# Kernel optimization log

Measured on AMD Instinct MI355X. Metric: run time of the kernel, lower is better.

The kernel has to match this reference:

```python
import jax, jax.numpy as jnp
import numpy as np

HIDDEN_NUMS = 512  # 2H = 1024, 4H = 2048


def setup_inputs() -> dict:
    key = jax.random.key(0)
    k1, k2, k3 = jax.random.split(key, 3)
    B, S, T, H2 = 32, 1024, 64, 2 * HIDDEN_NUMS
    target_hidden_states = jax.random.normal(k1, (B, T, H2), dtype=jnp.float32)
    hidden_states = jax.random.normal(k2, (B, S, H2), dtype=jnp.float32)
    # original uses RandomUniform(-0.01, 0.01)
    trans_W = jax.random.uniform(k3, (4 * HIDDEN_NUMS, H2), dtype=jnp.float32, minval=-0.01, maxval=0.01)
    trans_b = jnp.zeros((H2,), dtype=jnp.float32)
    return {
        'target_hidden_states': target_hidden_states,
        'hidden_states': hidden_states,
        'trans_W': trans_W,
        'trans_b': trans_b,
    }


def reference(target_hidden_states, hidden_states, trans_W, trans_b):
    # Vectorized form of the per-timestep while_loop (no cross-step recurrence):
    # scores[b,s,t] = <hidden[b,s], target[b,t]>
    scores = jnp.einsum('bsd,btd->bst', hidden_states, target_hidden_states)
    attn = jax.nn.softmax(scores, axis=-1)                      # (B, S, T)
    ti = jnp.einsum('bst,btd->bsd', attn, target_hidden_states)  # (B, S, 2H)
    cat = jnp.concatenate([hidden_states, ti], axis=-1)         # (B, S, 4H)
    hi_new = jnp.tanh(jnp.einsum('bsf,fd->bsd', cat, trans_W) + trans_b)
    return hi_new + hidden_states  # lf_layer residual
```

## Files before the change

kernel.cpp:

```cpp
#include <hip/hip_runtime.h>
#include <hip/hip_bf16.h>

#define BB 32
#define SS 1024
#define TT 64
#define HD 1024
#define FF 2048
#define MM (BB*SS)

typedef __attribute__((ext_vector_type(4))) float f32x4;
typedef __attribute__((ext_vector_type(8))) short bf16x8;

__device__ __forceinline__ unsigned short f2bf(float f) {
  __hip_bfloat16 h = __float2bfloat16(f);
  return __builtin_bit_cast(unsigned short, h);
}

__device__ __forceinline__ void gll16(const void* g, void* l) {
  __builtin_amdgcn_global_load_lds(
      (const __attribute__((address_space(1))) void*)g,
      (__attribute__((address_space(3))) void*)l, 16, 0, 0);
}

__global__ void cvt_bf16_kernel(const float* __restrict__ x,
                                unsigned short* __restrict__ y, int n4) {
  int stride = gridDim.x * blockDim.x;
  for (int i = blockIdx.x * blockDim.x + threadIdx.x; i < n4; i += stride) {
    float4 v = reinterpret_cast<const float4*>(x)[i];
    ushort4 o;
    o.x = f2bf(v.x); o.y = f2bf(v.y); o.z = f2bf(v.z); o.w = f2bf(v.w);
    reinterpret_cast<ushort4*>(y)[i] = o;
  }
}

__global__ void tcvt_kernel(const float* __restrict__ in,
                            unsigned short* __restrict__ out, int R, int C) {
  __shared__ float tile[32][33];
  const int bz = blockIdx.z;
  const float* ip = in + (size_t)bz * R * C;
  unsigned short* op = out + (size_t)bz * R * C;
  const int c0 = blockIdx.x * 32, r0 = blockIdx.y * 32;
  const int tx = threadIdx.x, ty = threadIdx.y;
#pragma unroll
  for (int j = 0; j < 4; ++j)
    tile[ty + j * 8][tx] = ip[(size_t)(r0 + ty + j * 8) * C + c0 + tx];
  __syncthreads();
#pragma unroll
  for (int j = 0; j < 4; ++j)
    op[(size_t)(c0 + ty + j * 8) * R + r0 + tx] = f2bf(tile[tx][ty + j * 8]);
}

__global__ __launch_bounds__(256) void attn_kernel(
    const unsigned short* __restrict__ hid_bf,
    const unsigned short* __restrict__ tgt_bf,
    const unsigned short* __restrict__ tgtT_bf,
    unsigned short* __restrict__ ti_bf)
{
  __shared__ unsigned short Qs[64 * 32];
  __shared__ unsigned short Ks[64 * 32];
  __shared__ unsigned short Ps[64 * 72];

  const int tid = threadIdx.x;
  const int w = tid >> 6, l = tid & 63;
  const int lrow = l & 15, lk = l >> 4;
  const int b = blockIdx.y;
  const int sbase = blockIdx.x * 64;

  const size_t hbase = ((size_t)b * SS + sbase) * HD;
  const size_t tbase = (size_t)b * TT * HD;
  const int srow = tid >> 2;
  const int scol = (tid & 3) * 8;

  f32x4 accs[4] = {};
  for (int kt = 0; kt < 32; ++kt) {
    const int kk = kt * 32;
    gll16(hid_bf + hbase + (size_t)srow * HD + kk + scol, Qs + w * 512);
    gll16(tgt_bf + tbase + (size_t)srow * HD + kk + scol, Ks + w * 512);
    __syncthreads();
    bf16x8 a = *reinterpret_cast<const bf16x8*>(&Qs[(w * 16 + lrow) * 32 + lk * 8]);
#pragma unroll
    for (int ct = 0; ct < 4; ++ct) {
      bf16x8 bb = *reinterpret_cast<const bf16x8*>(&Ks[(ct * 16 + lrow) * 32 + lk * 8]);
      accs[ct] = __builtin_amdgcn_mfma_f32_16x16x32_bf16(a, bb, accs[ct], 0, 0, 0);
    }
    __syncthreads();
  }

  float p[4][4];
#pragma unroll
  for (int j = 0; j < 4; ++j) {
    float mx = fmaxf(fmaxf(accs[0][j], accs[1][j]), fmaxf(accs[2][j], accs[3][j]));
#pragma unroll
    for (int d = 1; d < 16; d <<= 1) mx = fmaxf(mx, __shfl_xor(mx, d, 64));
    float sum = 0.f;
#pragma unroll
    for (int ct = 0; ct < 4; ++ct) { p[ct][j] = __expf(accs[ct][j] - mx); sum += p[ct][j]; }
#pragma unroll
    for (int d = 1; d < 16; d <<= 1) sum += __shfl_xor(sum, d, 64);
    float inv = 1.f / sum;
#pragma unroll
    for (int ct = 0; ct < 4; ++ct) p[ct][j] *= inv;
  }
#pragma unroll
  for (int j = 0; j < 4; ++j)
#pragma unroll
    for (int ct = 0; ct < 4; ++ct)
      Ps[(w * 16 + lk * 4 + j) * 72 + ct * 16 + lrow] = f2bf(p[ct][j]);
  __syncthreads();

  const size_t tTbase = (size_t)b * HD * TT;
  for (int chunk = 0; chunk < 16; ++chunk) {
    const int colbase = chunk * 64;
    f32x4 acco[4] = {};
#pragma unroll
    for (int kk2 = 0; kk2 < 2; ++kk2) {
      bf16x8 a = *reinterpret_cast<const bf16x8*>(&Ps[(w * 16 + lrow) * 72 + kk2 * 32 + lk * 8]);
#pragma unroll
      for (int ct = 0; ct < 4; ++ct) {
        const unsigned short* gp =
            tgtT_bf + tTbase + (size_t)(colbase + ct * 16 + lrow) * TT + kk2 * 32 + lk * 8;
        bf16x8 bb = *reinterpret_cast<const bf16x8*>(gp);
        acco[ct] = __builtin_amdgcn_mfma_f32_16x16x32_bf16(a, bb, acco[ct], 0, 0, 0);
      }
    }
#pragma unroll
    for (int ct = 0; ct < 4; ++ct)
#pragma unroll
      for (int j = 0; j < 4; ++j)
        ti_bf[hbase + (size_t)(w * 16 + lk * 4 + j) * HD + colbase + ct * 16 + lrow] =
            f2bf(acco[ct][j]);
  }
}


__global__ __launch_bounds__(512) void gemm_kernel(
    const unsigned short* __restrict__ hid_bf,
    const unsigned short* __restrict__ ti_bf,
    const unsigned short* __restrict__ Wt_bf,
    const float* __restrict__ bias,
    float* __restrict__ out)
{
  __shared__ unsigned short lds[65536];

  const int tid = threadIdx.x;
  const int w = tid >> 6, l = tid & 63;
  const int wm = w >> 2, wn = w & 3;
  const int lrow = l & 15, lk = l >> 4;

  const int orig = blockIdx.y * 4 + blockIdx.x;
  const int lid = (orig & 7) * 64 + (orig >> 3);
  const int nbase = (lid & 3) * 256;
  const int mbase = (lid >> 2) * 256;

  const int srow8 = w * 8 + (l >> 3);
  const int scol = ((l & 7) ^ (l >> 3)) << 3;

  const int ck0 = ((lk)     ^ (lrow & 7)) << 3;
  const int ck1 = ((4 + lk) ^ (lrow & 7)) << 3;

#define STAGE_A(s, bsel, h) do {                                               \
    const int k0_ = (s) * 64;                                                  \
    const unsigned short* p_ = (k0_ < 1024) ? (hid_bf + k0_)                   \
                                            : (ti_bf + (k0_ - 1024));          \
    _Pragma("unroll")                                                          \
    for (int rd_ = 0; rd_ < 2; ++rd_)                                          \
      gll16(p_ + (size_t)(mbase + (h) * 128 + rd_ * 64 + srow8) * HD + scol,   \
            lds + (bsel) * 32768 + (h) * 8192 + rd_ * 4096 + w * 512);         \
  } while (0)

#define STAGE_B(s, bsel, h) do {                                               \
    const int k0_ = (s) * 64;                                                  \
    _Pragma("unroll")                                                          \
    for (int rd_ = 0; rd_ < 2; ++rd_)                                          \
      gll16(Wt_bf + (size_t)(nbase + (h) * 128 + rd_ * 64 + srow8) * FF        \
                  + k0_ + scol,                                                \
            lds + (bsel) * 32768 + 16384 + (h) * 8192 + rd_ * 4096 + w * 512); \
  } while (0)

#define PH_MID do {                                                            \
    __builtin_amdgcn_s_barrier();                                              \
    __builtin_amdgcn_s_setprio(1);                                             \
  } while (0)

#define PH_END do {                                                            \
    __builtin_amdgcn_s_setprio(0);                                             \
    __builtin_amdgcn_sched_barrier(0);                                         \
    __builtin_amdgcn_s_barrier();                                              \
  } while (0)

  f32x4 acc[8][4] = {};
  bf16x8 aR[4][2], bR[4][2];

  STAGE_A(0, 0, 0); STAGE_A(0, 0, 1);
  STAGE_B(0, 0, 0); STAGE_B(0, 0, 1);
  STAGE_B(1, 1, 0); STAGE_B(1, 1, 1);
  asm volatile("s_waitcnt vmcnt(4)" ::: "memory");
  __builtin_amdgcn_sched_barrier(0);
  __builtin_amdgcn_s_barrier();

#define TILE(tt, c) do {                                                       \
    const int sa_ = ((tt) + 1 > 31) ? 31 : (tt) + 1;                           \
    const int sb_ = ((tt) + 2 > 31) ? 31 : (tt) + 2;                           \
    const int abase_ = (c) * 32768 + wm * 8192 + lrow * 64;                    \
    const int bbase_ = (c) * 32768 + 16384 + (wn >> 1) * 8192                  \
                       + ((wn & 1) * 64 + lrow) * 64;                          \
         \
    _Pragma("unroll")                                                          \
    for (int m_ = 0; m_ < 4; ++m_) {                                           \
      aR[m_][0] = *(const bf16x8*)(lds + abase_ + m_ * 1024 + ck0);            \
      aR[m_][1] = *(const bf16x8*)(lds + abase_ + m_ * 1024 + ck1);            \
    }                                                                          \
    _Pragma("unroll")                                                          \
    for (int n_ = 0; n_ < 2; ++n_) {                                           \
      bR[n_][0] = *(const bf16x8*)(lds + bbase_ + n_ * 1024 + ck0);            \
      bR[n_][1] = *(const bf16x8*)(lds + bbase_ + n_ * 1024 + ck1);            \
    }                                                                          \
    STAGE_A(sa_, 1 - (c), 0);                                                  \
    PH_MID;                                                                    \
    _Pragma("unroll")                                                          \
    for (int m_ = 0; m_ < 4; ++m_)                                             \
      _Pragma("unroll")                                                        \
      for (int n_ = 0; n_ < 2; ++n_) {                                         \
        acc[m_][n_] = __builtin_amdgcn_mfma_f32_16x16x32_bf16(                 \
            aR[m_][0], bR[n_][0], acc[m_][n_], 0, 0, 0);                       \
        acc[m_][n_] = __builtin_amdgcn_mfma_f32_16x16x32_bf16(                 \
            aR[m_][1], bR[n_][1], acc[m_][n_], 0, 0, 0);                       \
      }                                                                        \
    PH_END;                                                                    \
                  \
    _Pragma("unroll")                                                          \
    for (int n_ = 2; n_ < 4; ++n_) {                                           \
      bR[n_][0] = *(const bf16x8*)(lds + bbase_ + n_ * 1024 + ck0);            \
      bR[n_][1] = *(const bf16x8*)(lds + bbase_ + n_ * 1024 + ck1);            \
    }                                                                          \
    STAGE_A(sa_, 1 - (c), 1);                                                  \
    PH_MID;                                                                    \
    _Pragma("unroll")                                                          \
    for (int m_ = 0; m_ < 4; ++m_)                                             \
      _Pragma("unroll")                                                        \
      for (int n_ = 2; n_ < 4; ++n_) {                                         \
        acc[m_][n_] = __builtin_amdgcn_mfma_f32_16x16x32_bf16(                 \
            aR[m_][0], bR[n_][0], acc[m_][n_], 0, 0, 0);                       \
        acc[m_][n_] = __builtin_amdgcn_mfma_f32_16x16x32_bf16(                 \
            aR[m_][1], bR[n_][1], acc[m_][n_], 0, 0, 0);                       \
      }                                                                        \
    PH_END;                                                                    \
     \
    _Pragma("unroll")                                                          \
    for (int m_ = 0; m_ < 4; ++m_) {                                           \
      aR[m_][0] = *(const bf16x8*)(lds + abase_ + (m_ + 4) * 1024 + ck0);      \
      aR[m_][1] = *(const bf16x8*)(lds + abase_ + (m_ + 4) * 1024 + ck1);      \
    }                                                                          \
    STAGE_B(sb_, (c), 0);                                                      \
    PH_MID;                                                                    \
    _Pragma("unroll")                                                          \
    for (int m_ = 0; m_ < 4; ++m_)                                             \
      _Pragma("unroll")                                                        \
      for (int n_ = 0; n_ < 2; ++n_) {                                         \
        acc[m_ + 4][n_] = __builtin_amdgcn_mfma_f32_16x16x32_bf16(             \
            aR[m_][0], bR[n_][0], acc[m_ + 4][n_], 0, 0, 0);                   \
        acc[m_ + 4][n_] = __builtin_amdgcn_mfma_f32_16x16x32_bf16(             \
            aR[m_][1], bR[n_][1], acc[m_ + 4][n_], 0, 0, 0);                   \
      }                                                                        \
    PH_END;                                                                    \
       \
    STAGE_B(sb_, (c), 1);                                                      \
    PH_MID;                                                                    \
    _Pragma("unroll")                                                          \
    for (int m_ = 0; m_ < 4; ++m_)                                             \
      _Pragma("unroll")                                                        \
      for (int n_ = 2; n_ < 4; ++n_) {                                         \
        acc[m_ + 4][n_] = __builtin_amdgcn_mfma_f32_16x16x32_bf16(             \
            aR[m_][0], bR[n_][0], acc[m_ + 4][n_], 0, 0, 0);                   \
        acc[m_ + 4][n_] = __builtin_amdgcn_mfma_f32_16x16x32_bf16(             \
            aR[m_][1], bR[n_][1], acc[m_ + 4][n_], 0, 0, 0);                   \
      }                                                                        \
    __builtin_amdgcn_s_setprio(0);                                             \
    asm volatile("s_waitcnt vmcnt(4)" ::: "memory");                           \
    __builtin_amdgcn_sched_barrier(0);                                         \
    __builtin_amdgcn_s_barrier();                                              \
  } while (0)

  for (int tt = 0; tt < 32; tt += 2) {
    TILE(tt, 0);
    TILE(tt + 1, 1);
  }
#undef TILE
#undef PH_MID
#undef PH_END
#undef STAGE_A
#undef STAGE_B

#pragma unroll
  for (int m = 0; m < 8; ++m) {
    const int row = mbase + wm * 128 + m * 16 + lk * 4;
#pragma unroll
    for (int n = 0; n < 4; ++n) {
      const int col = nbase + wn * 64 + n * 16 + lrow;
      const float bv = bias[col];
#pragma unroll
      for (int j = 0; j < 4; ++j) {
        float x = acc[m][n][j] + bv;
        float xc = fminf(fmaxf(x, -15.f), 15.f);
        float e2 = __expf(2.f * xc);
        float th = (e2 - 1.f) / (e2 + 1.f);
        size_t oi = (size_t)(row + j) * HD + col;
        unsigned int u = ((unsigned int)hid_bf[oi]) << 16;
        out[oi] = th + __builtin_bit_cast(float, u);
      }
    }
  }
}

extern "C" void kernel_launch(void* const* d_in, const int* in_sizes, int n_in,
                              void* d_out, int out_size, void* d_ws, size_t ws_size,
                              hipStream_t stream) {
  const float* tgt  = (const float*)d_in[0];
  const float* hid  = (const float*)d_in[1];
  const float* W    = (const float*)d_in[2];
  const float* bias = (const float*)d_in[3];
  float* out = (float*)d_out;

  char* ws = (char*)d_ws;
  unsigned short* hid_bf  = (unsigned short*)(ws);
  unsigned short* ti_bf   = (unsigned short*)(ws + 67108864);
  unsigned short* tgt_bf  = (unsigned short*)(ws + 134217728);
  unsigned short* tgtT_bf = (unsigned short*)(ws + 138412032);
  unsigned short* Wt_bf   = (unsigned short*)(ws + 142606336);

  cvt_bf16_kernel<<<2048, 256, 0, stream>>>(hid, hid_bf, (BB * SS * HD) / 4);
  cvt_bf16_kernel<<<512, 256, 0, stream>>>(tgt, tgt_bf, (BB * TT * HD) / 4);
  tcvt_kernel<<<dim3(HD / 32, TT / 32, BB), dim3(32, 8), 0, stream>>>(tgt, tgtT_bf, TT, HD);
  tcvt_kernel<<<dim3(HD / 32, FF / 32, 1), dim3(32, 8), 0, stream>>>(W, Wt_bf, FF, HD);
  attn_kernel<<<dim3(SS / 64, BB), 256, 0, stream>>>(hid_bf, tgt_bf, tgtT_bf, ti_bf);
  gemm_kernel<<<dim3(HD / 128 / 2, MM / 256), 512, 0, stream>>>(hid_bf, ti_bf, Wt_bf, bias, out);
}
```

Measured before the change: 245.0 us.

## Fuse hidden-state bf16 conversion into attention kernel and use 32x32 MFMA in GEMM

The attention kernel now reads fp32 hidden states directly, converts them to bf16 in registers, writes them into LDS and also stores the bf16 copy to global memory for the GEMM. This removes the separate conversion pass over the large hidden tensor, and the next K-slice is prefetched in registers. The projection GEMM switches from 16x16x32 to 32x32x16 bf16 MFMA with restructured register fragments and fewer barrier phases per tile. The cost is more register pressure and a different LDS read pattern that may change bank-conflict behaviour.

```diff
diff --git a/kernel.cpp b/kernel.cpp
--- a/kernel.cpp
+++ b/kernel.cpp
@@ -9,7 +9,9 @@
 #define MM (BB*SS)
 
 typedef __attribute__((ext_vector_type(4))) float f32x4;
+typedef __attribute__((ext_vector_type(16))) float f32x16;
 typedef __attribute__((ext_vector_type(8))) short bf16x8;
+typedef __attribute__((ext_vector_type(8))) unsigned short u16x8;
 
 __device__ __forceinline__ unsigned short f2bf(float f) {
   __hip_bfloat16 h = __float2bfloat16(f);
@@ -51,7 +53,8 @@
 }
 
 __global__ __launch_bounds__(256) void attn_kernel(
-    const unsigned short* __restrict__ hid_bf,
+    const float* __restrict__ hid_f32,
+    unsigned short* __restrict__ hid_bf,
     const unsigned short* __restrict__ tgt_bf,
     const unsigned short* __restrict__ tgtT_bf,
     unsigned short* __restrict__ ti_bf)
@@ -71,19 +74,31 @@
   const int srow = tid >> 2;
   const int scol = (tid & 3) * 8;
 
+  const float* gq = hid_f32 + hbase + (size_t)srow * HD + scol;
+  float4 ga = *reinterpret_cast<const float4*>(gq);
+  float4 gb = *reinterpret_cast<const float4*>(gq + 4);
+
   f32x4 accs[4] = {};
   for (int kt = 0; kt < 32; ++kt) {
     const int kk = kt * 32;
-    gll16(hid_bf + hbase + (size_t)srow * HD + kk + scol, Qs + w * 512);
+    __syncthreads();
+    u16x8 pk;
+    pk[0] = f2bf(ga.x); pk[1] = f2bf(ga.y); pk[2] = f2bf(ga.z); pk[3] = f2bf(ga.w);
+    pk[4] = f2bf(gb.x); pk[5] = f2bf(gb.y); pk[6] = f2bf(gb.z); pk[7] = f2bf(gb.w);
+    *reinterpret_cast<u16x8*>(&Qs[tid * 8]) = pk;
+    *reinterpret_cast<u16x8*>(&hid_bf[hbase + (size_t)srow * HD + kk + scol]) = pk;
     gll16(tgt_bf + tbase + (size_t)srow * HD + kk + scol, Ks + w * 512);
     __syncthreads();
+    if (kt < 31) {
+      ga = *reinterpret_cast<const float4*>(gq + kk + 32);
+      gb = *reinterpret_cast<const float4*>(gq + kk + 36);
+    }
     bf16x8 a = *reinterpret_cast<const bf16x8*>(&Qs[(w * 16 + lrow) * 32 + lk * 8]);
 #pragma unroll
     for (int ct = 0; ct < 4; ++ct) {
       bf16x8 bb = *reinterpret_cast<const bf16x8*>(&Ks[(ct * 16 + lrow) * 32 + lk * 8]);
       accs[ct] = __builtin_amdgcn_mfma_f32_16x16x32_bf16(a, bb, accs[ct], 0, 0, 0);
     }
-    __syncthreads();
   }
 
   float p[4][4];
@@ -145,7 +160,7 @@
   const int tid = threadIdx.x;
   const int w = tid >> 6, l = tid & 63;
   const int wm = w >> 2, wn = w & 3;
-  const int lrow = l & 15, lk = l >> 4;
+  const int lr = l & 31, lh = l >> 5;
 
   const int orig = blockIdx.y * 4 + blockIdx.x;
   const int lid = (orig & 7) * 64 + (orig >> 3);
@@ -155,8 +170,11 @@
   const int srow8 = w * 8 + (l >> 3);
   const int scol = ((l & 7) ^ (l >> 3)) << 3;
 
-  const int ck0 = ((lk)     ^ (lrow & 7)) << 3;
-  const int ck1 = ((4 + lk) ^ (lrow & 7)) << 3;
+  const int abase0 = wm * 8192 + lr * 64;
+  const int bbase0 = 16384 + (wn >> 1) * 8192 + ((wn & 1) * 64 + lr) * 64;
+  int ck[4];
+#pragma unroll
+  for (int s = 0; s < 4; ++s) ck[s] = (((2 * s + lh) ^ (lr & 7)) << 3);
 
 #define STAGE_A(s, bsel, h) do {                                               \
     const int k0_ = (s) * 64;                                                  \
@@ -177,19 +195,8 @@
             lds + (bsel) * 32768 + 16384 + (h) * 8192 + rd_ * 4096 + w * 512); \
   } while (0)
 
-#define PH_MID do {                                                            \
-    __builtin_amdgcn_s_barrier();                                              \
-    __builtin_amdgcn_s_setprio(1);                                             \
-  } while (0)
-
-#define PH_END do {                                                            \
-    __builtin_amdgcn_s_setprio(0);                                             \
-    __builtin_amdgcn_sched_barrier(0);                                         \
-    __builtin_amdgcn_s_barrier();                                              \
-  } while (0)
-
-  f32x4 acc[8][4] = {};
-  bf16x8 aR[4][2], bR[4][2];
+  f32x16 acc[4][2] = {};
+  bf16x8 aR[2][4], bR[2][4];
 
   STAGE_A(0, 0, 0); STAGE_A(0, 0, 1);
   STAGE_B(0, 0, 0); STAGE_B(0, 0, 1);
@@ -201,80 +208,51 @@
 #define TILE(tt, c) do {                                                       \
     const int sa_ = ((tt) + 1 > 31) ? 31 : (tt) + 1;                           \
     const int sb_ = ((tt) + 2 > 31) ? 31 : (tt) + 2;                           \
-    const int abase_ = (c) * 32768 + wm * 8192 + lrow * 64;                    \
-    const int bbase_ = (c) * 32768 + 16384 + (wn >> 1) * 8192                  \
-                       + ((wn & 1) * 64 + lrow) * 64;                          \
-         \
-    _Pragma("unroll")                                                          \
-    for (int m_ = 0; m_ < 4; ++m_) {                                           \
-      aR[m_][0] = *(const bf16x8*)(lds + abase_ + m_ * 1024 + ck0);            \
-      aR[m_][1] = *(const bf16x8*)(lds + abase_ + m_ * 1024 + ck1);            \
-    }                                                                          \
-    _Pragma("unroll")                                                          \
-    for (int n_ = 0; n_ < 2; ++n_) {                                           \
-      bR[n_][0] = *(const bf16x8*)(lds + bbase_ + n_ * 1024 + ck0);            \
-      bR[n_][1] = *(const bf16x8*)(lds + bbase_ + n_ * 1024 + ck1);            \
-    }                                                                          \
+    const unsigned short* L_ = lds + (c) * 32768;                              \
+      \
+    _Pragma("unroll")                                                          \
+    for (int mb_ = 0; mb_ < 2; ++mb_)                                          \
+      _Pragma("unroll")                                                        \
+      for (int s_ = 0; s_ < 4; ++s_)                                           \
+        aR[mb_][s_] = *(const bf16x8*)(L_ + abase0 + mb_ * 2048 + ck[s_]);     \
+    _Pragma("unroll")                                                          \
+    for (int nb_ = 0; nb_ < 2; ++nb_)                                          \
+      _Pragma("unroll")                                                        \
+      for (int s_ = 0; s_ < 4; ++s_)                                           \
+        bR[nb_][s_] = *(const bf16x8*)(L_ + bbase0 + nb_ * 2048 + ck[s_]);     \
     STAGE_A(sa_, 1 - (c), 0);                                                  \
-    PH_MID;                                                                    \
-    _Pragma("unroll")                                                          \
-    for (int m_ = 0; m_ < 4; ++m_)                                             \
-      _Pragma("unroll")                                                        \
-      for (int n_ = 0; n_ < 2; ++n_) {                                         \
-        acc[m_][n_] = __builtin_amdgcn_mfma_f32_16x16x32_bf16(                 \
-            aR[m_][0], bR[n_][0], acc[m_][n_], 0, 0, 0);                       \
-        acc[m_][n_] = __builtin_amdgcn_mfma_f32_16x16x32_bf16(                 \
-            aR[m_][1], bR[n_][1], acc[m_][n_], 0, 0, 0);                       \
-      }                                                                        \
-    PH_END;                                                                    \
-                  \
-    _Pragma("unroll")                                                          \
-    for (int n_ = 2; n_ < 4; ++n_) {                                           \
-      bR[n_][0] = *(const bf16x8*)(lds + bbase_ + n_ * 1024 + ck0);            \
-      bR[n_][1] = *(const bf16x8*)(lds + bbase_ + n_ * 1024 + ck1);            \
-    }                                                                          \
     STAGE_A(sa_, 1 - (c), 1);                                                  \
-    PH_MID;                                                                    \
-    _Pragma("unroll")                                                          \
-    for (int m_ = 0; m_ < 4; ++m_)                                             \
-      _Pragma("unroll")                                                        \
-      for (int n_ = 2; n_ < 4; ++n_) {                                         \
-        acc[m_][n_] = __builtin_amdgcn_mfma_f32_16x16x32_bf16(                 \
-            aR[m_][0], bR[n_][0], acc[m_][n_], 0, 0, 0);                       \
-        acc[m_][n_] = __builtin_amdgcn_mfma_f32_16x16x32_bf16(                 \
-            aR[m_][1], bR[n_][1], acc[m_][n_], 0, 0, 0);                       \
-      }                                                                        \
-    PH_END;                                                                    \
-     \
-    _Pragma("unroll")                                                          \
-    for (int m_ = 0; m_ < 4; ++m_) {                                           \
-      aR[m_][0] = *(const bf16x8*)(lds + abase_ + (m_ + 4) * 1024 + ck0);      \
-      aR[m_][1] = *(const bf16x8*)(lds + abase_ + (m_ + 4) * 1024 + ck1);      \
-    }                                                                          \
+    __builtin_amdgcn_s_barrier();                                              \
+    __builtin_amdgcn_s_setprio(1);                                             \
+    _Pragma("unroll")                                                          \
+    for (int s_ = 0; s_ < 4; ++s_)                                             \
+      _Pragma("unroll")                                                        \
+      for (int mb_ = 0; mb_ < 2; ++mb_)                                        \
+        _Pragma("unroll")                                                      \
+        for (int nb_ = 0; nb_ < 2; ++nb_)                                      \
+          acc[mb_][nb_] = __builtin_amdgcn_mfma_f32_32x32x16_bf16(             \
+              aR[mb_][s_], bR[nb_][s_], acc[mb_][nb_], 0, 0, 0);               \
+    __builtin_amdgcn_s_setprio(0);                                             \
+    __builtin_amdgcn_sched_barrier(0);                                         \
+    __builtin_amdgcn_s_barrier();                                              \
+       \
+    _Pragma("unroll")                                                          \
+    for (int mb_ = 0; mb_ < 2; ++mb_)                                          \
+      _Pragma("unroll")                                                        \
+      for (int s_ = 0; s_ < 4; ++s_)                                           \
+        aR[mb_][s_] = *(const bf16x8*)(L_ + abase0 + (mb_ + 2) * 2048 + ck[s_]); \
     STAGE_B(sb_, (c), 0);                                                      \
-    PH_MID;                                                                    \
-    _Pragma("unroll")                                                          \
-    for (int m_ = 0; m_ < 4; ++m_)                                             \
-      _Pragma("unroll")                                                        \
-      for (int n_ = 0; n_ < 2; ++n_) {                                         \
-        acc[m_ + 4][n_] = __builtin_amdgcn_mfma_f32_16x16x32_bf16(             \
-            aR[m_][0], bR[n_][0], acc[m_ + 4][n_], 0, 0, 0);                   \
-        acc[m_ + 4][n_] = __builtin_amdgcn_mfma_f32_16x16x32_bf16(             \
-            aR[m_][1], bR[n_][1], acc[m_ + 4][n_], 0, 0, 0);                   \
-      }                                                                        \
-    PH_END;                                                                    \
-       \
     STAGE_B(sb_, (c), 1);                                                      \
-    PH_MID;                                                                    \
-    _Pragma("unroll")                                                          \
-    for (int m_ = 0; m_ < 4; ++m_)                                             \
-      _Pragma("unroll")                                                        \
-      for (int n_ = 2; n_ < 4; ++n_) {                                         \
-        acc[m_ + 4][n_] = __builtin_amdgcn_mfma_f32_16x16x32_bf16(             \
-            aR[m_][0], bR[n_][0], acc[m_ + 4][n_], 0, 0, 0);                   \
-        acc[m_ + 4][n_] = __builtin_amdgcn_mfma_f32_16x16x32_bf16(             \
-            aR[m_][1], bR[n_][1], acc[m_ + 4][n_], 0, 0, 0);                   \
-      }                                                                        \
+    __builtin_amdgcn_s_barrier();                                              \
+    __builtin_amdgcn_s_setprio(1);                                             \
+    _Pragma("unroll")                                                          \
+    for (int s_ = 0; s_ < 4; ++s_)                                             \
+      _Pragma("unroll")                                                        \
+      for (int mb_ = 0; mb_ < 2; ++mb_)                                        \
+        _Pragma("unroll")                                                      \
+        for (int nb_ = 0; nb_ < 2; ++nb_)                                      \
+          acc[mb_ + 2][nb_] = __builtin_amdgcn_mfma_f32_32x32x16_bf16(         \
+              aR[mb_][s_], bR[nb_][s_], acc[mb_ + 2][nb_], 0, 0, 0);           \
     __builtin_amdgcn_s_setprio(0);                                             \
     asm volatile("s_waitcnt vmcnt(4)" ::: "memory");                           \
     __builtin_amdgcn_sched_barrier(0);                                         \
@@ -286,25 +264,23 @@
     TILE(tt + 1, 1);
   }
 #undef TILE
-#undef PH_MID
-#undef PH_END
 #undef STAGE_A
 #undef STAGE_B
 
 #pragma unroll
-  for (int m = 0; m < 8; ++m) {
-    const int row = mbase + wm * 128 + m * 16 + lk * 4;
-#pragma unroll
-    for (int n = 0; n < 4; ++n) {
-      const int col = nbase + wn * 64 + n * 16 + lrow;
+  for (int mb = 0; mb < 4; ++mb) {
+#pragma unroll
+    for (int nb = 0; nb < 2; ++nb) {
+      const int col = nbase + wn * 64 + nb * 32 + lr;
       const float bv = bias[col];
 #pragma unroll
-      for (int j = 0; j < 4; ++j) {
-        float x = acc[m][n][j] + bv;
+      for (int r = 0; r < 16; ++r) {
+        const int row = mbase + wm * 128 + mb * 32 + (r & 3) + 8 * (r >> 2) + 4 * lh;
+        float x = acc[mb][nb][r] + bv;
         float xc = fminf(fmaxf(x, -15.f), 15.f);
         float e2 = __expf(2.f * xc);
         float th = (e2 - 1.f) / (e2 + 1.f);
-        size_t oi = (size_t)(row + j) * HD + col;
+        size_t oi = (size_t)row * HD + col;
         unsigned int u = ((unsigned int)hid_bf[oi]) << 16;
         out[oi] = th + __builtin_bit_cast(float, u);
       }
@@ -328,10 +304,9 @@
   unsigned short* tgtT_bf = (unsigned short*)(ws + 138412032);
   unsigned short* Wt_bf   = (unsigned short*)(ws + 142606336);
 
-  cvt_bf16_kernel<<<2048, 256, 0, stream>>>(hid, hid_bf, (BB * SS * HD) / 4);
   cvt_bf16_kernel<<<512, 256, 0, stream>>>(tgt, tgt_bf, (BB * TT * HD) / 4);
   tcvt_kernel<<<dim3(HD / 32, TT / 32, BB), dim3(32, 8), 0, stream>>>(tgt, tgtT_bf, TT, HD);
   tcvt_kernel<<<dim3(HD / 32, FF / 32, 1), dim3(32, 8), 0, stream>>>(W, Wt_bf, FF, HD);
-  attn_kernel<<<dim3(SS / 64, BB), 256, 0, stream>>>(hid_bf, tgt_bf, tgtT_bf, ti_bf);
+  attn_kernel<<<dim3(SS / 64, BB), 256, 0, stream>>>(hid, hid_bf, tgt_bf, tgtT_bf, ti_bf);
   gemm_kernel<<<dim3(HD / 128 / 2, MM / 256), 512, 0, stream>>>(hid_bf, ti_bf, Wt_bf, bias, out);
 }
```

New measurement: 260.9 us. 1.07x slower.

## Fuse hidden-state bf16 conversion into attention kernel and drop LDS staging

Applied to the files above, without the earlier changes.

Removes the standalone fp32-to-bf16 conversion of hidden_states. The attention kernel now writes the bf16 copy that the GEMM needs and converts Q fragments from fp32 in registers. The QK^T loop also drops its LDS staging and barriers and loads Q and K fragments directly from global memory. This saves a kernel launch and one pass over hidden_states, but the attention kernel now reads the fp32 tile twice (convert pass plus Q loads) and makes uncoalesced direct global fragment loads.

```diff
diff --git a/kernel.cpp b/kernel.cpp
--- a/kernel.cpp
+++ b/kernel.cpp
@@ -10,6 +10,7 @@
 
 typedef __attribute__((ext_vector_type(4))) float f32x4;
 typedef __attribute__((ext_vector_type(8))) short bf16x8;
+typedef __attribute__((ext_vector_type(8))) unsigned short u16x8;
 
 __device__ __forceinline__ unsigned short f2bf(float f) {
   __hip_bfloat16 h = __float2bfloat16(f);
@@ -51,13 +52,12 @@
 }
 
 __global__ __launch_bounds__(256) void attn_kernel(
-    const unsigned short* __restrict__ hid_bf,
+    const float* __restrict__ hid_f32,
+    unsigned short* __restrict__ hid_bf,
     const unsigned short* __restrict__ tgt_bf,
     const unsigned short* __restrict__ tgtT_bf,
     unsigned short* __restrict__ ti_bf)
 {
-  __shared__ unsigned short Qs[64 * 32];
-  __shared__ unsigned short Ks[64 * 32];
   __shared__ unsigned short Ps[64 * 72];
 
   const int tid = threadIdx.x;
@@ -65,25 +65,41 @@
   const int lrow = l & 15, lk = l >> 4;
   const int b = blockIdx.y;
   const int sbase = blockIdx.x * 64;
-
   const size_t hbase = ((size_t)b * SS + sbase) * HD;
-  const size_t tbase = (size_t)b * TT * HD;
-  const int srow = tid >> 2;
-  const int scol = (tid & 3) * 8;
+
+  {
+    const float* src = hid_f32 + hbase;
+    unsigned short* dst = hid_bf + hbase;
+    for (int i = 0; i < 32; ++i) {
+      const int idx = i * 2048 + tid * 8;
+      float4 v0 = *reinterpret_cast<const float4*>(src + idx);
+      float4 v1 = *reinterpret_cast<const float4*>(src + idx + 4);
+      u16x8 pk;
+      pk[0] = f2bf(v0.x); pk[1] = f2bf(v0.y); pk[2] = f2bf(v0.z); pk[3] = f2bf(v0.w);
+      pk[4] = f2bf(v1.x); pk[5] = f2bf(v1.y); pk[6] = f2bf(v1.z); pk[7] = f2bf(v1.w);
+      *reinterpret_cast<u16x8*>(dst + idx) = pk;
+    }
+  }
+
+  const int qrow = w * 16 + lrow;
+  const float* qp = hid_f32 + hbase + (size_t)qrow * HD + lk * 8;
+  const unsigned short* kp = tgt_bf + (size_t)b * TT * HD + (size_t)lrow * HD + lk * 8;
 
   f32x4 accs[4] = {};
   for (int kt = 0; kt < 32; ++kt) {
     const int kk = kt * 32;
-    gll16(hid_bf + hbase + (size_t)srow * HD + kk + scol, Qs + w * 512);
-    gll16(tgt_bf + tbase + (size_t)srow * HD + kk + scol, Ks + w * 512);
-    __syncthreads();
-    bf16x8 a = *reinterpret_cast<const bf16x8*>(&Qs[(w * 16 + lrow) * 32 + lk * 8]);
+    float4 f0 = *reinterpret_cast<const float4*>(qp + kk);
+    float4 f1 = *reinterpret_cast<const float4*>(qp + kk + 4);
+    bf16x8 a;
+    a[0] = (short)f2bf(f0.x); a[1] = (short)f2bf(f0.y);
+    a[2] = (short)f2bf(f0.z); a[3] = (short)f2bf(f0.w);
+    a[4] = (short)f2bf(f1.x); a[5] = (short)f2bf(f1.y);
+    a[6] = (short)f2bf(f1.z); a[7] = (short)f2bf(f1.w);
 #pragma unroll
     for (int ct = 0; ct < 4; ++ct) {
-      bf16x8 bb = *reinterpret_cast<const bf16x8*>(&Ks[(ct * 16 + lrow) * 32 + lk * 8]);
+      bf16x8 bb = *reinterpret_cast<const bf16x8*>(kp + (size_t)ct * 16 * HD + kk);
       accs[ct] = __builtin_amdgcn_mfma_f32_16x16x32_bf16(a, bb, accs[ct], 0, 0, 0);
     }
-    __syncthreads();
   }
 
   float p[4][4];
@@ -328,10 +344,9 @@
   unsigned short* tgtT_bf = (unsigned short*)(ws + 138412032);
   unsigned short* Wt_bf   = (unsigned short*)(ws + 142606336);
 
-  cvt_bf16_kernel<<<2048, 256, 0, stream>>>(hid, hid_bf, (BB * SS * HD) / 4);
   cvt_bf16_kernel<<<512, 256, 0, stream>>>(tgt, tgt_bf, (BB * TT * HD) / 4);
   tcvt_kernel<<<dim3(HD / 32, TT / 32, BB), dim3(32, 8), 0, stream>>>(tgt, tgtT_bf, TT, HD);
   tcvt_kernel<<<dim3(HD / 32, FF / 32, 1), dim3(32, 8), 0, stream>>>(W, Wt_bf, FF, HD);
-  attn_kernel<<<dim3(SS / 64, BB), 256, 0, stream>>>(hid_bf, tgt_bf, tgtT_bf, ti_bf);
+  attn_kernel<<<dim3(SS / 64, BB), 256, 0, stream>>>(hid, hid_bf, tgt_bf, tgtT_bf, ti_bf);
   gemm_kernel<<<dim3(HD / 128 / 2, MM / 256), 512, 0, stream>>>(hid_bf, ti_bf, Wt_bf, bias, out);
 }
```

New measurement: 273.0 us. 1.11x slower.
